# Kernel tuning notes

Measured on AMD Instinct MI355X. Metric: run time of the kernel, lower is better.

Reference implementation:

```python
import jax, jax.numpy as jnp
import numpy as np

N = 32768; D = 384; P = 3; CORR_D = 2 * 49 * P * P  # 882
G_KK = 4096; G_JK = 512
EPS = 1e-3  # LayerNorm eps in the torch module

FLOAT_NAMES = ("net","inp","corr","corr_w1","corr_b1","corr_w2","corr_b2","corr_ln_g","corr_ln_b","corr_w3","corr_b3","norm_g","norm_b","c1_w1","c1_b1","c1_w2","c1_b2","c2_w1","c2_b1","c2_w2","c2_b2","kk_fw","kk_fb","kk_gw","kk_gb","kk_hw","kk_hb","ij_fw","ij_fb","ij_gw","ij_gb","ij_hw","ij_hb","g_ln1_g","g_ln1_b","g1_gw","g1_gb","g1_r1w","g1_r1b","g1_r2w","g1_r2b","g_ln2_g","g_ln2_b","g2_gw","g2_gb","g2_r1w","g2_r1b","g2_r2w","g2_r2b","d_w","d_b","w_w","w_b")

def _ln(x, g, b):
    m = jnp.mean(x, -1, keepdims=True)
    v = jnp.mean((x - m) ** 2, -1, keepdims=True)
    return (x - m) * jax.lax.rsqrt(v + EPS) * g + b

def _mlp2(x, w1, b1, w2, b2):
    return jax.nn.relu(x @ w1 + b1) @ w2 + b2

def _gated_residual(x, gw, gb, r1w, r1b, r2w, r2b):
    gate = jax.nn.sigmoid(x @ gw + gb)
    res = jax.nn.relu(x @ r1w + r1b) @ r2w + r2b
    return x + gate * res

def _soft_agg(x, jx, fw, fb, gw, gb, hw, hb, num_groups):
    # x: [N, D]; jx: [N] group ids -> group-wise softmax weighted sum
    logits = x @ gw + gb
    feats = x @ fw + fb
    gmax = jax.ops.segment_max(logits, jx, num_segments=num_groups)
    e = jnp.exp(logits - gmax[jx])
    den = jax.ops.segment_sum(e, jx, num_segments=num_groups)
    w = e / (den[jx] + 1e-12)
    y = jax.ops.segment_sum(feats * w, jx, num_segments=num_groups)
    return (y @ hw + hb)[jx]

def _forward(p, nix, njx, ukk, ujk):
    # corr encoder MLP
    h = jax.nn.relu(p["corr"] @ p["corr_w1"] + p["corr_b1"]) @ p["corr_w2"] + p["corr_b2"]
    h = jax.nn.relu(_ln(h, p["corr_ln_g"], p["corr_ln_b"])) @ p["corr_w3"] + p["corr_b3"]
    net = p["net"] + p["inp"] + h
    net = _ln(net, p["norm_g"], p["norm_b"])
    mask_ix = (nix >= 0).astype(net.dtype).reshape(1, -1, 1)
    mask_jx = (njx >= 0).astype(net.dtype).reshape(1, -1, 1)
    net = net + _mlp2(mask_ix * net[:, nix], p["c1_w1"], p["c1_b1"], p["c1_w2"], p["c1_b2"])
    net = net + _mlp2(mask_jx * net[:, njx], p["c2_w1"], p["c2_b1"], p["c2_w2"], p["c2_b2"])
    net = net + _soft_agg(net[0], ukk, p["kk_fw"], p["kk_fb"], p["kk_gw"], p["kk_gb"], p["kk_hw"], p["kk_hb"], G_KK)[None]
    net = net + _soft_agg(net[0], ujk, p["ij_fw"], p["ij_fb"], p["ij_gw"], p["ij_gb"], p["ij_hw"], p["ij_hb"], G_JK)[None]
    net = _ln(net, p["g_ln1_g"], p["g_ln1_b"])
    net = _gated_residual(net, p["g1_gw"], p["g1_gb"], p["g1_r1w"], p["g1_r1b"], p["g1_r2w"], p["g1_r2b"])
    net = _ln(net, p["g_ln2_g"], p["g_ln2_b"])
    net = _gated_residual(net, p["g2_gw"], p["g2_gb"], p["g2_r1w"], p["g2_r1b"], p["g2_r2w"], p["g2_r2b"])
    r = jax.nn.relu(net)
    d = r @ p["d_w"] + p["d_b"]               # GradClip is identity in forward
    w = jax.nn.sigmoid(r @ p["w_w"] + p["w_b"])
    return net, d, w

def setup_inputs() -> dict:
    key = jax.random.key(0)
    it = iter(jax.random.split(key, 64))
    def pr(*shape):
        return jax.random.normal(next(it), shape, dtype=jnp.float32) * 0.02
    z = lambda *s: jnp.zeros(s, jnp.float32)
    o = lambda *s: jnp.ones(s, jnp.float32)
    inp = {
        "net": jax.random.normal(next(it), (1, N, D), dtype=jnp.float32),
        "inp": jax.random.normal(next(it), (1, N, D), dtype=jnp.float32),
        "corr": jax.random.normal(next(it), (1, N, CORR_D), dtype=jnp.float32),
        "nix": jax.random.randint(next(it), (N,), 0, N),
        "njx": jax.random.randint(next(it), (N,), 0, N),
        "ukk": jax.random.randint(next(it), (N,), 0, G_KK),
        "ujk": jax.random.randint(next(it), (N,), 0, G_JK),
        "corr_w1": pr(CORR_D, D), "corr_b1": z(D), "corr_w2": pr(D, D), "corr_b2": z(D),
        "corr_ln_g": o(D), "corr_ln_b": z(D), "corr_w3": pr(D, D), "corr_b3": z(D),
        "norm_g": o(D), "norm_b": z(D),
        "c1_w1": pr(D, D), "c1_b1": z(D), "c1_w2": pr(D, D), "c1_b2": z(D),
        "c2_w1": pr(D, D), "c2_b1": z(D), "c2_w2": pr(D, D), "c2_b2": z(D),
        "kk_fw": pr(D, D), "kk_fb": z(D), "kk_gw": pr(D, D), "kk_gb": z(D), "kk_hw": pr(D, D), "kk_hb": z(D),
        "ij_fw": pr(D, D), "ij_fb": z(D), "ij_gw": pr(D, D), "ij_gb": z(D), "ij_hw": pr(D, D), "ij_hb": z(D),
        "g_ln1_g": o(D), "g_ln1_b": z(D),
        "g1_gw": pr(D, D), "g1_gb": z(D), "g1_r1w": pr(D, D), "g1_r1b": z(D), "g1_r2w": pr(D, D), "g1_r2b": z(D),
        "g_ln2_g": o(D), "g_ln2_b": z(D),
        "g2_gw": pr(D, D), "g2_gb": z(D), "g2_r1w": pr(D, D), "g2_r1b": z(D), "g2_r2w": pr(D, D), "g2_r2b": z(D),
        "d_w": pr(D, 2), "d_b": z(2), "w_w": pr(D, 2), "w_b": z(2),
    }
    return inp

def reference(net, inp, corr, corr_w1, corr_b1, corr_w2, corr_b2, corr_ln_g, corr_ln_b, corr_w3, corr_b3, norm_g, norm_b, c1_w1, c1_b1, c1_w2, c1_b2, c2_w1, c2_b1, c2_w2, c2_b2, kk_fw, kk_fb, kk_gw, kk_gb, kk_hw, kk_hb, ij_fw, ij_fb, ij_gw, ij_gb, ij_hw, ij_hb, g_ln1_g, g_ln1_b, g1_gw, g1_gb, g1_r1w, g1_r1b, g1_r2w, g1_r2b, g_ln2_g, g_ln2_b, g2_gw, g2_gb, g2_r1w, g2_r1b, g2_r2w, g2_r2b, d_w, d_b, w_w, w_b, nix, njx, ukk, ujk):
    loc = locals()
    fl = {k: loc[k] for k in FLOAT_NAMES}
    return _forward(fl, nix, njx, ukk, ujk)
```

## Files before the change

### kernel.cpp

```cpp
#include <hip/hip_runtime.h>
#include <hip/hip_bf16.h>
#include <math.h>

#define NR 32768
#define DD 384
#define CDM 882
#define CDMP 896

typedef float f4 __attribute__((ext_vector_type(4)));
typedef float f32x4 __attribute__((ext_vector_type(4)));
typedef __bf16 bf16x8 __attribute__((ext_vector_type(8)));

__device__ inline f4 ld4(const float* p) { f4 v; __builtin_memcpy(&v, p, 16); return v; }
__device__ inline void st4(float* p, f4 v) { __builtin_memcpy(p, &v, 16); }
__device__ inline bf16x8 ld8h(const __bf16* p) { bf16x8 v; __builtin_memcpy(&v, p, 16); return v; }
__device__ inline void st8h(__bf16* p, bf16x8 v) { __builtin_memcpy(p, &v, 16); }

__device__ inline void gl_lds16(const void* g, void* l) {
  __builtin_amdgcn_global_load_lds(
      (const __attribute__((address_space(1))) void*)g,
      (__attribute__((address_space(3))) void*)l, 16, 0, 0);
}

__device__ inline float gred16(float v) {
#pragma unroll
  for (int o = 1; o < 16; o <<= 1) v += __shfl_xor(v, o, 64);
  return v;
}

__device__ inline int xcd_swz(int orig, int nwg) {
  int q = nwg >> 3, r = nwg & 7, xcd = orig & 7, lid = orig >> 3;
  return (xcd < r ? xcd * (q + 1) : r * (q + 1) + (xcd - r) * q) + lid;
}

struct WPtrs { const float* w[19]; };

__global__ __launch_bounds__(256) void trans_all_k(WPtrs P, __bf16* __restrict__ dst) {
  int wi = blockIdx.y;
  const float* W = P.w[wi];
  int i = blockIdx.x * 256 + threadIdx.x;
  if (wi < 18) {
    if (i >= DD * DD) return;
    int n = i / DD, k = i - n * DD;
    dst[(size_t)wi * DD * DD + i] = (__bf16)W[(size_t)k * DD + n];
  } else {
    if (i >= DD * CDMP) return;
    int n = i / CDMP, k = i - n * CDMP;
    dst[(size_t)18 * DD * DD + i] = (k < CDM) ? (__bf16)W[(size_t)k * DD + n] : (__bf16)0.f;
  }
}

struct GP {
  const void* A; const __bf16* WT; const float* bias; __bf16* OUT;
  const __bf16* XRES; const __bf16* GIN;
  const float* p0; const float* p1; const float* p2; const float* p3;
  float* fout; const float* net32; const float* inp32;
  const int* idx; const __bf16* zpage; int M; int K; int Kr;
};

template <int EPI>
__device__ __forceinline__ void epilogue(const GP& gp, f32x4 (&acc)[4][6],
                                         __bf16* sm, int m0, int w, int lane) {
  const int fr = lane & 15, fq = lane >> 4;
  const int wr = (w >> 2) * 64, wc = (w & 3) * 96;
  const int nw = w & 3;
  float bcol[6];
#pragma unroll
  for (int ni = 0; ni < 6; ++ni) bcol[ni] = gp.bias[wc + ni * 16 + fr];
#pragma unroll
  for (int mi = 0; mi < 4; ++mi)
#pragma unroll
    for (int ni = 0; ni < 6; ++ni)
#pragma unroll
      for (int j = 0; j < 4; ++j) acc[mi][ni][j] += bcol[ni];

  if constexpr (EPI <= 2) {
#pragma unroll
    for (int mi = 0; mi < 4; ++mi)
#pragma unroll
      for (int ni = 0; ni < 6; ++ni) {
        int col = wc + ni * 16 + fr;
#pragma unroll
        for (int j = 0; j < 4; ++j) {
          int row = m0 + wr + mi * 16 + fq * 4 + j;
          size_t o = (size_t)row * DD + col;
          float v = acc[mi][ni][j];
          if constexpr (EPI == 0) gp.OUT[o] = (__bf16)v;
          else if constexpr (EPI == 1) gp.OUT[o] = (__bf16)fmaxf(v, 0.f);
          else gp.OUT[o] = (__bf16)((float)gp.XRES[o] + v);
        }
      }
  } else {
    if constexpr (EPI == 5) {
#pragma unroll
      for (int mi = 0; mi < 4; ++mi)
#pragma unroll
        for (int ni = 0; ni < 6; ++ni) {
          int col = wc + ni * 16 + fr;
#pragma unroll
          for (int j = 0; j < 4; ++j) {
            int row = m0 + wr + mi * 16 + fq * 4 + j;
            size_t o = (size_t)row * DD + col;
            acc[mi][ni][j] += gp.net32[o] + gp.inp32[o];
          }
        }
    }
    if constexpr (EPI == 6 || EPI == 7) {
#pragma unroll
      for (int mi = 0; mi < 4; ++mi)
#pragma unroll
        for (int ni = 0; ni < 6; ++ni) {
          int col = wc + ni * 16 + fr;
#pragma unroll
          for (int j = 0; j < 4; ++j) {
            int row = m0 + wr + mi * 16 + fq * 4 + j;
            size_t o = (size_t)row * DD + col;
            float gl = (float)gp.GIN[o];
            float sg = 1.f / (1.f + expf(-gl));
            acc[mi][ni][j] = (float)gp.XRES[o] + sg * acc[mi][ni][j];
          }
        }
    }
    __syncthreads();
    if constexpr (EPI != 7) {
      float s1[4][4], s2[4][4];
#pragma unroll
      for (int mi = 0; mi < 4; ++mi)
#pragma unroll
        for (int j = 0; j < 4; ++j) { s1[mi][j] = 0.f; s2[mi][j] = 0.f; }
#pragma unroll
      for (int mi = 0; mi < 4; ++mi)
#pragma unroll
        for (int ni = 0; ni < 6; ++ni)
#pragma unroll
          for (int j = 0; j < 4; ++j) {
            float v = acc[mi][ni][j];
            s1[mi][j] += v;
            s2[mi][j] += v * v;
          }
#pragma unroll
      for (int o = 1; o < 16; o <<= 1)
#pragma unroll
        for (int mi = 0; mi < 4; ++mi)
#pragma unroll
          for (int j = 0; j < 4; ++j) {
            s1[mi][j] += __shfl_xor(s1[mi][j], o, 64);
            s2[mi][j] += __shfl_xor(s2[mi][j], o, 64);
          }
      float* lsum = (float*)sm;
      float* lsq = lsum + 512;
      if (fr == 0) {
#pragma unroll
        for (int mi = 0; mi < 4; ++mi)
#pragma unroll
          for (int j = 0; j < 4; ++j) {
            int rr = wr + mi * 16 + fq * 4 + j;
            lsum[rr * 4 + nw] = s1[mi][j];
            lsq[rr * 4 + nw] = s2[mi][j];
          }
      }
      __syncthreads();
      float mn[4][4], rs[4][4];
#pragma unroll
      for (int mi = 0; mi < 4; ++mi)
#pragma unroll
        for (int j = 0; j < 4; ++j) {
          int rr = wr + mi * 16 + fq * 4 + j;
          float S1 = lsum[rr * 4] + lsum[rr * 4 + 1] + lsum[rr * 4 + 2] + lsum[rr * 4 + 3];
          float S2 = lsq[rr * 4] + lsq[rr * 4 + 1] + lsq[rr * 4 + 2] + lsq[rr * 4 + 3];
          float m = S1 * (1.f / 384.f);
          float va = S2 * (1.f / 384.f) - m * m;
          mn[mi][j] = m;
          rs[mi][j] = rsqrtf(va + 1e-3f);
        }
#pragma unroll
      for (int ni = 0; ni < 6; ++ni) {
        int col = wc + ni * 16 + fr;
        float gg = gp.p0[col], bb = gp.p1[col];
#pragma unroll
        for (int mi = 0; mi < 4; ++mi)
#pragma unroll
          for (int j = 0; j < 4; ++j) {
            int row = m0 + wr + mi * 16 + fq * 4 + j;
            float y = (acc[mi][ni][j] - mn[mi][j]) * rs[mi][j] * gg + bb;
            if constexpr (EPI == 4) y = fmaxf(y, 0.f);
            gp.OUT[(size_t)row * DD + col] = (__bf16)y;
          }
      }
    } else {
      float c0[6], c1[6], c2[6], c3[6];
#pragma unroll
      for (int ni = 0; ni < 6; ++ni) {
        int col = wc + ni * 16 + fr;
        c0[ni] = gp.p0[2 * col];
        c1[ni] = gp.p0[2 * col + 1];
        c2[ni] = gp.p2[2 * col];
        c3[ni] = gp.p2[2 * col + 1];
      }
      float dt[4][4][4];
#pragma unroll
      for (int mi = 0; mi < 4; ++mi)
#pragma unroll
        for (int j = 0; j < 4; ++j)
#pragma unroll
          for (int q = 0; q < 4; ++q) dt[mi][j][q] = 0.f;
#pragma unroll
      for (int mi = 0; mi < 4; ++mi)
#pragma unroll
        for (int ni = 0; ni < 6; ++ni) {
          int col = wc + ni * 16 + fr;
#pragma unroll
          for (int j = 0; j < 4; ++j) {
            int row = m0 + wr + mi * 16 + fq * 4 + j;
            float v = acc[mi][ni][j];
            gp.fout[(size_t)row * DD + col] = v;
            float r = fmaxf(v, 0.f);
            dt[mi][j][0] += r * c0[ni];
            dt[mi][j][1] += r * c1[ni];
            dt[mi][j][2] += r * c2[ni];
            dt[mi][j][3] += r * c3[ni];
          }
        }
#pragma unroll
      for (int o = 1; o < 16; o <<= 1)
#pragma unroll
        for (int mi = 0; mi < 4; ++mi)
#pragma unroll
          for (int j = 0; j < 4; ++j)
#pragma unroll
            for (int q = 0; q < 4; ++q)
              dt[mi][j][q] += __shfl_xor(dt[mi][j][q], o, 64);
      float* lt = (float*)sm;
      if (fr == 0) {
#pragma unroll
        for (int mi = 0; mi < 4; ++mi)
#pragma unroll
          for (int j = 0; j < 4; ++j) {
            int rr = wr + mi * 16 + fq * 4 + j;
#pragma unroll
            for (int q = 0; q < 4; ++q) lt[(rr * 4 + nw) * 4 + q] = dt[mi][j][q];
          }
      }
      __syncthreads();
      if (nw == 0 && fr == 0) {
        float* fd = gp.fout + (size_t)NR * DD;
        float* fw = fd + (size_t)NR * 2;
#pragma unroll
        for (int mi = 0; mi < 4; ++mi)
#pragma unroll
          for (int j = 0; j < 4; ++j) {
            int rr = wr + mi * 16 + fq * 4 + j;
            int row = m0 + rr;
            float T[4];
#pragma unroll
            for (int q = 0; q < 4; ++q)
              T[q] = lt[(rr * 4 + 0) * 4 + q] + lt[(rr * 4 + 1) * 4 + q] +
                     lt[(rr * 4 + 2) * 4 + q] + lt[(rr * 4 + 3) * 4 + q];
            fd[2 * row] = T[0] + gp.p1[0];
            fd[2 * row + 1] = T[1] + gp.p1[1];
            fw[2 * row] = 1.f / (1.f + expf(-(T[2] + gp.p3[0])));
            fw[2 * row + 1] = 1.f / (1.f + expf(-(T[3] + gp.p3[1])));
          }
      }
    }
  }
}

__device__ __forceinline__ void mfma_block(const __bf16* As, const __bf16* Bs,
                                           f32x4 (&acc)[4][6], int wr, int wc,
                                           int fr, int fq) {
#pragma unroll
  for (int kk2 = 0; kk2 < 2; ++kk2) {
    bf16x8 af[4];
    bf16x8 bv[6];
#pragma unroll
    for (int mi = 0; mi < 4; ++mi) {
      int rr = wr + mi * 16 + fr;
      af[mi] = *reinterpret_cast<const bf16x8*>(
          &As[rr * 64 + (((fq + kk2 * 4) ^ (rr & 7)) << 3)]);
    }
#pragma unroll
    for (int ni = 0; ni < 6; ++ni) {
      int rr = wc + ni * 16 + fr;
      bv[ni] = *reinterpret_cast<const bf16x8*>(
          &Bs[rr * 64 + (((fq + kk2 * 4) ^ (rr & 7)) << 3)]);
    }
#pragma unroll
    for (int mi = 0; mi < 4; ++mi)
#pragma unroll
      for (int ni = 0; ni < 6; ++ni)
        acc[mi][ni] = __builtin_amdgcn_mfma_f32_16x16x32_bf16(af[mi], bv[ni],
                                                              acc[mi][ni], 0, 0, 0);
  }
}

__device__ __forceinline__ void zero_acc(f32x4 (&acc)[4][6]) {
#pragma unroll
  for (int a = 0; a < 4; ++a)
#pragma unroll
    for (int b = 0; b < 6; ++b)
#pragma unroll
      for (int j = 0; j < 4; ++j) acc[a][b][j] = 0.f;
}

__device__ __forceinline__ void phase1_run(const GP& gp, f32x4 (&acc)[4][6],
                                           __bf16* sm, int m0, int t, int w,
                                           int lane, int NT) {
  const int fr = lane & 15, fq = lane >> 4;
  const int wr = (w >> 2) * 64, wc = (w & 3) * 96;
  const int K = gp.K;
  const __bf16* aptr[2];
  int aadv[2];
  const __bf16* bptr[6];
#pragma unroll
  for (int j = 0; j < 2; ++j) {
    int rloc = w * 16 + j * 8 + (lane >> 3);
    int cch = (lane & 7) ^ (rloc & 7);
    int ar = gp.idx ? gp.idx[m0 + rloc] : (m0 + rloc);
    if (ar >= 0) { aptr[j] = (const __bf16*)gp.A + (size_t)ar * K + cch * 8; aadv[j] = 64; }
    else { aptr[j] = gp.zpage; aadv[j] = 0; }
  }
#pragma unroll
  for (int j = 0; j < 6; ++j) {
    int rloc = w * 48 + j * 8 + (lane >> 3);
    int cch = (lane & 7) ^ (rloc & 7);
    bptr[j] = gp.WT + (size_t)rloc * K + cch * 8;
  }
  auto stageG = [&](int buf) {
    __bf16* As = sm + buf * 32768;
    __bf16* Bs = As + 8192;
#pragma unroll
    for (int j = 0; j < 2; ++j) {
      gl_lds16(aptr[j], &As[(w * 16 + j * 8) * 64]);
      aptr[j] += aadv[j];
    }
#pragma unroll
    for (int j = 0; j < 6; ++j) {
      gl_lds16(bptr[j], &Bs[(w * 48 + j * 8) * 64]);
      bptr[j] += 64;
    }
  };
  stageG(0);
  int buf = 0;
  for (int tt = 0; tt < NT; ++tt) {
    if (tt + 1 < NT) {
      stageG(buf ^ 1);
      asm volatile("s_waitcnt vmcnt(8)" ::: "memory");
    } else {
      asm volatile("s_waitcnt vmcnt(0)" ::: "memory");
    }
    __builtin_amdgcn_s_barrier();
    __builtin_amdgcn_sched_barrier(0);
    mfma_block(sm + buf * 32768, sm + buf * 32768 + 8192, acc, wr, wc, fr, fq);
    __builtin_amdgcn_s_barrier();
    __builtin_amdgcn_sched_barrier(0);
    buf ^= 1;
  }
}

template <int EPI, int AFP32>
__global__ __launch_bounds__(512, 1) void gemm_k(GP gp) {
  __shared__ __align__(16) __bf16 sm[2 * 32768];
  const int t = threadIdx.x;
  const int w = t >> 6, lane = t & 63;
  const int m0 = xcd_swz(blockIdx.x, gridDim.x) * 128;
  const int fr = lane & 15, fq = lane >> 4;
  const int wr = (w >> 2) * 64, wc = (w & 3) * 96;
  f32x4 acc[4][6];
  zero_acc(acc);
  if constexpr (AFP32) {
    const float* Af = (const float*)gp.A;
    const int K = gp.K, Kr = gp.Kr;
    const __bf16* bptr[6];
#pragma unroll
    for (int j = 0; j < 6; ++j) {
      int rloc = w * 48 + j * 8 + (lane >> 3);
      int cch = (lane & 7) ^ (rloc & 7);
      bptr[j] = gp.WT + (size_t)rloc * K + cch * 8;
    }
    const int NT = K >> 6;
    for (int tt = 0; tt < NT; ++tt) {
      if (tt) __syncthreads();
      __bf16* As = sm;
      __bf16* Bs = sm + 8192;
#pragma unroll
      for (int j = 0; j < 2; ++j) {
        int rr = (t >> 3) + 64 * j;
        int cc = t & 7;
        int kb = (tt << 6) + cc * 8;
        const float* ap = Af + (size_t)(m0 + rr) * Kr + kb;
        bf16x8 h;
        if (kb + 8 <= Kr) {
          f4 v0 = ld4(ap), v1 = ld4(ap + 4);
#pragma unroll
          for (int e = 0; e < 4; ++e) { h[e] = (__bf16)v0[e]; h[4 + e] = (__bf16)v1[e]; }
        } else {
#pragma unroll
          for (int e = 0; e < 8; ++e) h[e] = (kb + e < Kr) ? (__bf16)ap[e] : (__bf16)0.f;
        }
        *reinterpret_cast<bf16x8*>(&As[rr * 64 + ((cc ^ (rr & 7)) << 3)]) = h;
      }
#pragma unroll
      for (int j = 0; j < 6; ++j) {
        gl_lds16(bptr[j], &Bs[(w * 48 + j * 8) * 64]);
        bptr[j] += 64;
      }
      __syncthreads();
      mfma_block(sm, sm + 8192, acc, wr, wc, fr, fq);
    }
  } else {
    phase1_run(gp, acc, sm, m0, t, w, lane, gp.K >> 6);
  }
  epilogue<EPI>(gp, acc, sm, m0, w, lane);
}

template <int EPIA, int EPIB>
__global__ __launch_bounds__(512, 1) void gemm2_k(GP ga, GP gb) {
  __shared__ __align__(16) __bf16 sm[2 * 32768];
  const int t = threadIdx.x;
  const int w = t >> 6, lane = t & 63;
  int wg = xcd_swz(blockIdx.x, gridDim.x);
  const int role = wg >> 8;
  const int m0 = (wg & 255) * 128;
  const GP& gp = role ? gb : ga;
  f32x4 acc[4][6];
  zero_acc(acc);
  phase1_run(gp, acc, sm, m0, t, w, lane, gp.K >> 6);
  if (role == 0) epilogue<EPIA>(ga, acc, sm, m0, w, lane);
  else epilogue<EPIB>(gb, acc, sm, m0, w, lane);
}

__global__ __launch_bounds__(256) void ln_ag_k(const __bf16* __restrict__ X,
                                               const __bf16* __restrict__ z,
                                               const int* __restrict__ gid,
                                               const float* __restrict__ g,
                                               const float* __restrict__ b,
                                               __bf16* __restrict__ out) {
  int w = threadIdx.x >> 6, lane = threadIdx.x & 63;
  int s = lane & 15, qq = lane >> 4;
  int row = blockIdx.x * 16 + w * 4 + qq;
  int gr = gid[row];
  size_t base = (size_t)row * DD;
  size_t zbase = (size_t)gr * DD;
  float v[24];
#pragma unroll
  for (int i = 0; i < 3; ++i) {
    int col = (s + 16 * i) * 8;
    bf16x8 h = ld8h(X + base + col);
    bf16x8 zz = ld8h(z + zbase + col);
#pragma unroll
    for (int e = 0; e < 8; ++e) v[i * 8 + e] = (float)h[e] + (float)zz[e];
  }
  float sm = 0.f;
#pragma unroll
  for (int i = 0; i < 24; ++i) sm += v[i];
  sm = gred16(sm);
  float mean = sm * (1.f / 384.f);
  float qs = 0.f;
#pragma unroll
  for (int i = 0; i < 24; ++i) { float d = v[i] - mean; qs += d * d; }
  qs = gred16(qs);
  float rs = rsqrtf(qs * (1.f / 384.f) + 1e-3f);
#pragma unroll
  for (int i = 0; i < 3; ++i) {
    int col = (s + 16 * i) * 8;
    f4 g0 = ld4(g + col), g1 = ld4(g + col + 4);
    f4 b0 = ld4(b + col), b1 = ld4(b + col + 4);
    bf16x8 o;
#pragma unroll
    for (int e = 0; e < 4; ++e) {
      o[e] = (__bf16)((v[i * 8 + e] - mean) * rs * g0[e] + b0[e]);
      o[4 + e] = (__bf16)((v[i * 8 + 4 + e] - mean) * rs * g1[e] + b1[e]);
    }
    st8h(out + base + col, o);
  }
}

__global__ __launch_bounds__(256) void hist2_k(const int* __restrict__ ukk,
                                               const int* __restrict__ ujk,
                                               int* __restrict__ ckk,
                                               int* __restrict__ cij) {
  int i = blockIdx.x * 256 + threadIdx.x;
  atomicAdd(&ckk[ukk[i]], 1);
  atomicAdd(&cij[ujk[i]], 1);
}

__device__ inline void scan_body(const int* cnt, int* off, int* curb, int G, int* ls) {
  int t = threadIdx.x;
  int per = G / 256;
  int base = t * per;
  int s = 0;
  for (int i = 0; i < per; ++i) s += cnt[base + i];
  ls[t] = s;
  __syncthreads();
  for (int o = 1; o < 256; o <<= 1) {
    int v = (t >= o) ? ls[t - o] : 0;
    __syncthreads();
    ls[t] += v;
    __syncthreads();
  }
  int run = (t == 0) ? 0 : ls[t - 1];
  for (int i = 0; i < per; ++i) {
    off[base + i] = run;
    run += cnt[base + i];
    curb[base + i] = 0;
  }
  if (t == 255) off[G] = run;
}

__global__ __launch_bounds__(256) void scan2_k(const int* ckk, int* okk, int* qkk,
                                               const int* cij, int* oij, int* qij) {
  __shared__ int ls[256];
  if (blockIdx.x == 0) scan_body(ckk, okk, qkk, 4096, ls);
  else scan_body(cij, oij, qij, 512, ls);
}

__global__ __launch_bounds__(256) void scatter2_k(const int* __restrict__ ukk,
                                                  const int* __restrict__ ujk,
                                                  const int* __restrict__ okk,
                                                  int* __restrict__ qkk,
                                                  int* __restrict__ rkk,
                                                  const int* __restrict__ oij,
                                                  int* __restrict__ qij,
                                                  int* __restrict__ rij) {
  int i = blockIdx.x * 256 + threadIdx.x;
  int g1 = ukk[i];
  rkk[okk[g1] + atomicAdd(&qkk[g1], 1)] = i;
  int g2 = ujk[i];
  rij[oij[g2] + atomicAdd(&qij[g2], 1)] = i;
}

__global__ __launch_bounds__(384) void segagg_k(const __bf16* __restrict__ L,
                                                const __bf16* __restrict__ Ft,
                                                const int* __restrict__ rows,
                                                const int* __restrict__ off,
                                                float* __restrict__ yb) {
  int g = blockIdx.x;
  int c = threadIdx.x;
  int s = off[g], e = off[g + 1];
  float mx = -3.0e38f;
  for (int p = s; p < e; ++p) {
    int r = rows[p];
    mx = fmaxf(mx, (float)L[(size_t)r * DD + c]);
  }
  float num = 0.f, den = 0.f;
  for (int p = s; p < e; ++p) {
    int r = rows[p];
    float lv = (float)L[(size_t)r * DD + c];
    float fv = (float)Ft[(size_t)r * DD + c];
    float ev = expf(lv - mx);
    den += ev;
    num += fv * ev;
  }
  yb[(size_t)g * DD + c] = num / (den + 1e-12f);
}

__global__ __launch_bounds__(256) void addgather_k(__bf16* __restrict__ X,
                                                   const __bf16* __restrict__ z,
                                                   const int* __restrict__ gid) {
  int i = blockIdx.x * 256 + threadIdx.x;
  int row = i / 48, c = (i - row * 48) * 8;
  int g = gid[row];
  size_t lo = (size_t)row * DD + c;
  bf16x8 a = ld8h(X + lo);
  bf16x8 zz = ld8h(z + (size_t)g * DD + c);
  bf16x8 o;
#pragma unroll
  for (int e = 0; e < 8; ++e) o[e] = (__bf16)((float)a[e] + (float)zz[e]);
  st8h(X + lo, o);
}

extern "C" void kernel_launch(void* const* d_in, const int* in_sizes, int n_in,
                              void* d_out, int out_size, void* d_ws, size_t ws_size,
                              hipStream_t stream) {
  const float* in_net = (const float*)d_in[0];
  const float* in_inp = (const float*)d_in[1];
  const float* in_corr = (const float*)d_in[2];
  const int* nix = (const int*)d_in[3];
  const int* njx = (const int*)d_in[4];
  const int* ukk = (const int*)d_in[5];
  const int* ujk = (const int*)d_in[6];
  auto F = [&](int i) { return (const float*)d_in[i]; };

  constexpr size_t MiB = 1024 * 1024;
  constexpr size_t SZ_ACT = (size_t)NR * DD * 2;
  char* ws = (char*)d_ws;
  __bf16* T2b = (__bf16*)(ws);
  __bf16* Fb = (__bf16*)(ws + SZ_ACT);
  __bf16* zb = (__bf16*)(ws + 2 * SZ_ACT);
  float* yb = (float*)(ws + 2 * SZ_ACT + 3 * MiB);
  __bf16* T1b = (__bf16*)(ws + 60 * MiB);
  char* p = ws + 84 * MiB;
  int* rows_kk = (int*)p; p += (size_t)NR * 4;
  int* rows_ij = (int*)p; p += (size_t)NR * 4;
  int* off_kk = (int*)p; p += 8192 * 4;
  int* off_ij = (int*)p; p += 1024 * 4;
  int* cnt_kk = (int*)p; p += 4096 * 4;
  int* cnt_ij = (int*)p; p += 512 * 4;
  int* curb_kk = (int*)p; p += 4096 * 4;
  int* curb_ij = (int*)p; p += 512 * 4;
  __bf16* wt_all = (__bf16*)p; p += (size_t)18 * DD * DD * 2;
  __bf16* wt_corr1 = (__bf16*)p; p += (size_t)DD * CDMP * 2;
  __bf16* zpage = (__bf16*)p;

  const int widx[18] = {17, 19, 21, 23, 25, 27, 29, 31, 33, 35, 39, 41, 43, 47, 49, 51, 9, 13};
  WPtrs P;
  for (int i = 0; i < 18; ++i) P.w[i] = F(widx[i]);
  P.w[18] = F(7);
  auto WTp = [&](int i) { return wt_all + (size_t)i * DD * DD; };

  hipMemsetAsync(zpage, 0, 256, stream);
  hipMemsetAsync(cnt_kk, 0, 4096 * 4, stream);
  hipMemsetAsync(cnt_ij, 0, 512 * 4, stream);
  trans_all_k<<<dim3(1344, 19), 256, 0, stream>>>(P, wt_all);
  hist2_k<<<NR / 256, 256, 0, stream>>>(ukk, ujk, cnt_kk, cnt_ij);
  scan2_k<<<2, 256, 0, stream>>>(cnt_kk, off_kk, curb_kk, cnt_ij, off_ij, curb_ij);
  scatter2_k<<<NR / 256, 256, 0, stream>>>(ukk, ujk, off_kk, curb_kk, rows_kk,
                                           off_ij, curb_ij, rows_ij);

  auto mkGP = [&]() {
    GP g{};
    g.zpage = zpage;
    g.K = DD;
    g.Kr = DD;
    g.M = NR;
    return g;
  };

  auto launch = [&](int epi, int afp32, const GP& gp) {
    dim3 g(gp.M / 128), b(512);
    if (afp32) {
      if (epi == 1) gemm_k<1, 1><<<g, b, 0, stream>>>(gp);
      else gemm_k<0, 1><<<g, b, 0, stream>>>(gp);
      return;
    }
    switch (epi) {
      case 0: gemm_k<0, 0><<<g, b, 0, stream>>>(gp); break;
      case 1: gemm_k<1, 0><<<g, b, 0, stream>>>(gp); break;
      case 2: gemm_k<2, 0><<<g, b, 0, stream>>>(gp); break;
      case 4: gemm_k<4, 0><<<g, b, 0, stream>>>(gp); break;
      case 5: gemm_k<5, 0><<<g, b, 0, stream>>>(gp); break;
      case 6: gemm_k<6, 0><<<g, b, 0, stream>>>(gp); break;
      case 7: gemm_k<7, 0><<<g, b, 0, stream>>>(gp); break;
    }
  };
  auto launch2 = [&](int epib, const GP& ga, const GP& gb) {
    dim3 g(512), b(512);
    if (epib == 0) gemm2_k<0, 0><<<g, b, 0, stream>>>(ga, gb);
    else gemm2_k<0, 1><<<g, b, 0, stream>>>(ga, gb);
  };

  const int SEGB = NR * 48 / 256;

  {
    GP g = mkGP(); g.A = in_corr; g.WT = wt_corr1; g.bias = F(8); g.OUT = T1b;
    g.K = CDMP; g.Kr = CDM;
    launch(1, 1, g);
  }
  {
    GP g = mkGP(); g.A = T1b; g.WT = WTp(16); g.bias = F(10); g.OUT = T2b;
    g.p0 = F(11); g.p1 = F(12);
    launch(4, 0, g);
  }
  {
    GP g = mkGP(); g.A = T2b; g.WT = WTp(17); g.bias = F(14); g.OUT = T1b;
    g.p0 = F(15); g.p1 = F(16); g.net32 = in_net; g.inp32 = in_inp;
    launch(5, 0, g);
  }
  {
    GP g = mkGP(); g.A = T1b; g.WT = WTp(0); g.bias = F(18); g.OUT = T2b; g.idx = nix;
    launch(1, 0, g);
  }
  {
    GP g = mkGP(); g.A = T2b; g.WT = WTp(1); g.bias = F(20); g.OUT = Fb; g.XRES = T1b;
    launch(2, 0, g);
  }
  {
    GP g = mkGP(); g.A = Fb; g.WT = WTp(2); g.bias = F(22); g.OUT = T2b; g.idx = njx;
    launch(1, 0, g);
  }
  {
    GP g = mkGP(); g.A = T2b; g.WT = WTp(3); g.bias = F(24); g.OUT = T1b; g.XRES = Fb;
    launch(2, 0, g);
  }
  {
    GP ga = mkGP(); ga.A = T1b; ga.WT = WTp(5); ga.bias = F(28); ga.OUT = T2b;
    GP gb = mkGP(); gb.A = T1b; gb.WT = WTp(4); gb.bias = F(26); gb.OUT = Fb;
    launch2(0, ga, gb);
  }
  segagg_k<<<4096, 384, 0, stream>>>(T2b, Fb, rows_kk, off_kk, yb);
  {
    GP g = mkGP(); g.A = yb; g.WT = WTp(6); g.bias = F(30); g.OUT = zb; g.M = 4096;
    launch(0, 1, g);
  }
  addgather_k<<<SEGB, 256, 0, stream>>>(T1b, zb, ukk);
  {
    GP ga = mkGP(); ga.A = T1b; ga.WT = WTp(8); ga.bias = F(34); ga.OUT = T2b;
    GP gb = mkGP(); gb.A = T1b; gb.WT = WTp(7); gb.bias = F(32); gb.OUT = Fb;
    launch2(0, ga, gb);
  }
  segagg_k<<<512, 384, 0, stream>>>(T2b, Fb, rows_ij, off_ij, yb);
  {
    GP g = mkGP(); g.A = yb; g.WT = WTp(9); g.bias = F(36); g.OUT = zb; g.M = 512;
    launch(0, 1, g);
  }
  ln_ag_k<<<NR / 16, 256, 0, stream>>>(T1b, zb, ujk, F(37), F(38), T2b);
  {
    GP ga = mkGP(); ga.A = T2b; ga.WT = WTp(10); ga.bias = F(40); ga.OUT = Fb;
    GP gb = mkGP(); gb.A = T2b; gb.WT = WTp(11); gb.bias = F(42); gb.OUT = T1b;
    launch2(1, ga, gb);
  }
  {
    GP g = mkGP(); g.A = T1b; g.WT = WTp(12); g.bias = F(44); g.OUT = T2b;
    g.XRES = T2b; g.GIN = Fb; g.p0 = F(45); g.p1 = F(46);
    launch(6, 0, g);
  }
  {
    GP ga = mkGP(); ga.A = T2b; ga.WT = WTp(13); ga.bias = F(48); ga.OUT = Fb;
    GP gb = mkGP(); gb.A = T2b; gb.WT = WTp(14); gb.bias = F(50); gb.OUT = T1b;
    launch2(1, ga, gb);
  }
  {
    GP g = mkGP(); g.A = T1b; g.WT = WTp(15); g.bias = F(52);
    g.XRES = T2b; g.GIN = Fb; g.p0 = F(53); g.p1 = F(54); g.p2 = F(55); g.p3 = F(56);
    g.fout = (float*)d_out;
    launch(7, 0, g);
  }
}
```

Baseline: 628.4 us.

## Stage residual/gate tiles through LDS, precompute net+inp, split dual GEMM launches

Adds a kernel that sums net and inp into one bf16 buffer, so the corr-encoder epilogue reads a single bf16 residual instead of two fp32 tensors. Residual and gate epilogues now copy the tile into LDS with async global-to-LDS loads rather than doing strided per-element global reads, and the LayerNorm epilogue is restructured. The fused two-role gemm2 kernel is removed and replaced by two sequential single GEMM launches. This adds an extra elementwise pass and extra launches in exchange for more coalesced epilogue traffic.

```diff
diff --git a/kernel.cpp b/kernel.cpp
--- a/kernel.cpp
+++ b/kernel.cpp
@@ -12,7 +12,6 @@
 typedef __bf16 bf16x8 __attribute__((ext_vector_type(8)));
 
 __device__ inline f4 ld4(const float* p) { f4 v; __builtin_memcpy(&v, p, 16); return v; }
-__device__ inline void st4(float* p, f4 v) { __builtin_memcpy(p, &v, 16); }
 __device__ inline bf16x8 ld8h(const __bf16* p) { bf16x8 v; __builtin_memcpy(&v, p, 16); return v; }
 __device__ inline void st8h(__bf16* p, bf16x8 v) { __builtin_memcpy(p, &v, 16); }
 
@@ -31,6 +30,21 @@
 __device__ inline int xcd_swz(int orig, int nwg) {
   int q = nwg >> 3, r = nwg & 7, xcd = orig & 7, lid = orig >> 3;
   return (xcd < r ? xcd * (q + 1) : r * (q + 1) + (xcd - r) * q) + lid;
+}
+
+__global__ __launch_bounds__(256) void ni_k(const float* __restrict__ a,
+                                            const float* __restrict__ b,
+                                            __bf16* __restrict__ o) {
+  size_t base = ((size_t)blockIdx.x * 256 + threadIdx.x) * 8;
+  f4 a0 = ld4(a + base), a1 = ld4(a + base + 4);
+  f4 b0 = ld4(b + base), b1 = ld4(b + base + 4);
+  bf16x8 h;
+#pragma unroll
+  for (int e = 0; e < 4; ++e) {
+    h[e] = (__bf16)(a0[e] + b0[e]);
+    h[4 + e] = (__bf16)(a1[e] + b1[e]);
+  }
+  st8h(o + base, h);
 }
 
 struct WPtrs { const float* w[19]; };
@@ -54,13 +68,24 @@
   const void* A; const __bf16* WT; const float* bias; __bf16* OUT;
   const __bf16* XRES; const __bf16* GIN;
   const float* p0; const float* p1; const float* p2; const float* p3;
-  float* fout; const float* net32; const float* inp32;
-  const int* idx; const __bf16* zpage; int M; int K; int Kr;
+  float* fout; const int* idx; const __bf16* zpage; int M; int K; int Kr;
 };
+
+__device__ __forceinline__ void stage_tile(const __bf16* X, int m0, __bf16* sm, int t) {
+  const char* src = (const char*)(X + (size_t)m0 * DD);
+  char* dst = (char*)sm;
+#pragma unroll
+  for (int i = 0; i < 12; ++i) {
+    int ch = t + i * 512;
+    gl_lds16(src + (size_t)ch * 16, dst + ch * 16);
+  }
+  asm volatile("s_waitcnt vmcnt(0)" ::: "memory");
+  __builtin_amdgcn_s_barrier();
+}
 
 template <int EPI>
 __device__ __forceinline__ void epilogue(const GP& gp, f32x4 (&acc)[4][6],
-                                         __bf16* sm, int m0, int w, int lane) {
+                                         __bf16* sm, int m0, int w, int lane, int t) {
   const int fr = lane & 15, fq = lane >> 4;
   const int wr = (w >> 2) * 64, wc = (w & 3) * 96;
   const int nw = w & 3;
@@ -74,7 +99,7 @@
 #pragma unroll
       for (int j = 0; j < 4; ++j) acc[mi][ni][j] += bcol[ni];
 
-  if constexpr (EPI <= 2) {
+  if constexpr (EPI <= 1) {
 #pragma unroll
     for (int mi = 0; mi < 4; ++mi)
 #pragma unroll
@@ -86,43 +111,111 @@
           size_t o = (size_t)row * DD + col;
           float v = acc[mi][ni][j];
           if constexpr (EPI == 0) gp.OUT[o] = (__bf16)v;
-          else if constexpr (EPI == 1) gp.OUT[o] = (__bf16)fmaxf(v, 0.f);
-          else gp.OUT[o] = (__bf16)((float)gp.XRES[o] + v);
-        }
-      }
-  } else {
-    if constexpr (EPI == 5) {
-#pragma unroll
-      for (int mi = 0; mi < 4; ++mi)
+          else gp.OUT[o] = (__bf16)fmaxf(v, 0.f);
+        }
+      }
+  } else if constexpr (EPI == 4) {
+    __syncthreads();
+    float s1[4][4], s2[4][4];
+#pragma unroll
+    for (int mi = 0; mi < 4; ++mi)
+#pragma unroll
+      for (int j = 0; j < 4; ++j) { s1[mi][j] = 0.f; s2[mi][j] = 0.f; }
+#pragma unroll
+    for (int mi = 0; mi < 4; ++mi)
+#pragma unroll
+      for (int ni = 0; ni < 6; ++ni)
+#pragma unroll
+        for (int j = 0; j < 4; ++j) {
+          float v = acc[mi][ni][j];
+          s1[mi][j] += v;
+          s2[mi][j] += v * v;
+        }
+#pragma unroll
+    for (int o = 1; o < 16; o <<= 1)
+#pragma unroll
+      for (int mi = 0; mi < 4; ++mi)
+#pragma unroll
+        for (int j = 0; j < 4; ++j) {
+          s1[mi][j] += __shfl_xor(s1[mi][j], o, 64);
+          s2[mi][j] += __shfl_xor(s2[mi][j], o, 64);
+        }
+    float* lsum = (float*)sm;
+    float* lsq = lsum + 512;
+    if (fr == 0) {
+#pragma unroll
+      for (int mi = 0; mi < 4; ++mi)
+#pragma unroll
+        for (int j = 0; j < 4; ++j) {
+          int rr = wr + mi * 16 + fq * 4 + j;
+          lsum[rr * 4 + nw] = s1[mi][j];
+          lsq[rr * 4 + nw] = s2[mi][j];
+        }
+    }
+    __syncthreads();
+#pragma unroll
+    for (int mi = 0; mi < 4; ++mi)
+#pragma unroll
+      for (int j = 0; j < 4; ++j) {
+        int rr = wr + mi * 16 + fq * 4 + j;
+        float S1 = lsum[rr * 4] + lsum[rr * 4 + 1] + lsum[rr * 4 + 2] + lsum[rr * 4 + 3];
+        float S2 = lsq[rr * 4] + lsq[rr * 4 + 1] + lsq[rr * 4 + 2] + lsq[rr * 4 + 3];
+        float m = S1 * (1.f / 384.f);
+        float va = S2 * (1.f / 384.f) - m * m;
+        float rs = rsqrtf(va + 1e-3f);
 #pragma unroll
         for (int ni = 0; ni < 6; ++ni) {
           int col = wc + ni * 16 + fr;
+          float y = (acc[mi][ni][j] - m) * rs * gp.p0[col] + gp.p1[col];
+          gp.OUT[(size_t)(m0 + rr) * DD + col] = (__bf16)fmaxf(y, 0.f);
+        }
+      }
+  } else {
+    __syncthreads();
+    if constexpr (EPI == 6 || EPI == 7) {
+      stage_tile(gp.GIN, m0, sm, t);
+#pragma unroll
+      for (int mi = 0; mi < 4; ++mi)
+#pragma unroll
+        for (int ni = 0; ni < 6; ++ni) {
+          int col = wc + ni * 16 + fr;
+#pragma unroll
+          for (int j = 0; j < 4; ++j) {
+            int rr = wr + mi * 16 + fq * 4 + j;
+            float gl = (float)sm[rr * DD + col];
+            acc[mi][ni][j] *= 1.f / (1.f + expf(-gl));
+          }
+        }
+      __syncthreads();
+    }
+    stage_tile(gp.XRES, m0, sm, t);
+#pragma unroll
+    for (int mi = 0; mi < 4; ++mi)
+#pragma unroll
+      for (int ni = 0; ni < 6; ++ni) {
+        int col = wc + ni * 16 + fr;
+#pragma unroll
+        for (int j = 0; j < 4; ++j) {
+          int rr = wr + mi * 16 + fq * 4 + j;
+          acc[mi][ni][j] += (float)sm[rr * DD + col];
+        }
+      }
+    if constexpr (EPI == 2) {
+#pragma unroll
+      for (int mi = 0; mi < 4; ++mi)
+#pragma unroll
+        for (int ni = 0; ni < 6; ++ni) {
+          int col = wc + ni * 16 + fr;
 #pragma unroll
           for (int j = 0; j < 4; ++j) {
             int row = m0 + wr + mi * 16 + fq * 4 + j;
-            size_t o = (size_t)row * DD + col;
-            acc[mi][ni][j] += gp.net32[o] + gp.inp32[o];
-          }
-        }
-    }
-    if constexpr (EPI == 6 || EPI == 7) {
-#pragma unroll
-      for (int mi = 0; mi < 4; ++mi)
-#pragma unroll
-        for (int ni = 0; ni < 6; ++ni) {
-          int col = wc + ni * 16 + fr;
-#pragma unroll
-          for (int j = 0; j < 4; ++j) {
-            int row = m0 + wr + mi * 16 + fq * 4 + j;
-            size_t o = (size_t)row * DD + col;
-            float gl = (float)gp.GIN[o];
-            float sg = 1.f / (1.f + expf(-gl));
-            acc[mi][ni][j] = (float)gp.XRES[o] + sg * acc[mi][ni][j];
-          }
-        }
+            gp.OUT[(size_t)row * DD + col] = (__bf16)acc[mi][ni][j];
+          }
+        }
+      return;
     }
     __syncthreads();
-    if constexpr (EPI != 7) {
+    if constexpr (EPI == 5 || EPI == 6) {
       float s1[4][4], s2[4][4];
 #pragma unroll
       for (int mi = 0; mi < 4; ++mi)
@@ -160,7 +253,6 @@
           }
       }
       __syncthreads();
-      float mn[4][4], rs[4][4];
 #pragma unroll
       for (int mi = 0; mi < 4; ++mi)
 #pragma unroll
@@ -170,23 +262,14 @@
           float S2 = lsq[rr * 4] + lsq[rr * 4 + 1] + lsq[rr * 4 + 2] + lsq[rr * 4 + 3];
           float m = S1 * (1.f / 384.f);
           float va = S2 * (1.f / 384.f) - m * m;
-          mn[mi][j] = m;
-          rs[mi][j] = rsqrtf(va + 1e-3f);
-        }
-#pragma unroll
-      for (int ni = 0; ni < 6; ++ni) {
-        int col = wc + ni * 16 + fr;
-        float gg = gp.p0[col], bb = gp.p1[col];
-#pragma unroll
-        for (int mi = 0; mi < 4; ++mi)
-#pragma unroll
-          for (int j = 0; j < 4; ++j) {
-            int row = m0 + wr + mi * 16 + fq * 4 + j;
-            float y = (acc[mi][ni][j] - mn[mi][j]) * rs[mi][j] * gg + bb;
-            if constexpr (EPI == 4) y = fmaxf(y, 0.f);
-            gp.OUT[(size_t)row * DD + col] = (__bf16)y;
-          }
-      }
+          float rs = rsqrtf(va + 1e-3f);
+#pragma unroll
+          for (int ni = 0; ni < 6; ++ni) {
+            int col = wc + ni * 16 + fr;
+            float y = (acc[mi][ni][j] - m) * rs * gp.p0[col] + gp.p1[col];
+            gp.OUT[(size_t)(m0 + rr) * DD + col] = (__bf16)y;
+          }
+        }
     } else {
       float c0[6], c1[6], c2[6], c3[6];
 #pragma unroll
@@ -408,26 +491,11 @@
       __syncthreads();
       mfma_block(sm, sm + 8192, acc, wr, wc, fr, fq);
     }
+    __syncthreads();
   } else {
     phase1_run(gp, acc, sm, m0, t, w, lane, gp.K >> 6);
   }
-  epilogue<EPI>(gp, acc, sm, m0, w, lane);
-}
-
-template <int EPIA, int EPIB>
-__global__ __launch_bounds__(512, 1) void gemm2_k(GP ga, GP gb) {
-  __shared__ __align__(16) __bf16 sm[2 * 32768];
-  const int t = threadIdx.x;
-  const int w = t >> 6, lane = t & 63;
-  int wg = xcd_swz(blockIdx.x, gridDim.x);
-  const int role = wg >> 8;
-  const int m0 = (wg & 255) * 128;
-  const GP& gp = role ? gb : ga;
-  f32x4 acc[4][6];
-  zero_acc(acc);
-  phase1_run(gp, acc, sm, m0, t, w, lane, gp.K >> 6);
-  if (role == 0) epilogue<EPIA>(ga, acc, sm, m0, w, lane);
-  else epilogue<EPIB>(gb, acc, sm, m0, w, lane);
+  epilogue<EPI>(gp, acc, sm, m0, w, lane, t);
 }
 
 __global__ __launch_bounds__(256) void ln_ag_k(const __bf16* __restrict__ X,
@@ -601,7 +669,8 @@
   int* curb_ij = (int*)p; p += 512 * 4;
   __bf16* wt_all = (__bf16*)p; p += (size_t)18 * DD * DD * 2;
   __bf16* wt_corr1 = (__bf16*)p; p += (size_t)DD * CDMP * 2;
-  __bf16* zpage = (__bf16*)p;
+  __bf16* zpage = (__bf16*)p; p += 4096;
+  __bf16* NI = (__bf16*)p;
 
   const int widx[18] = {17, 19, 21, 23, 25, 27, 29, 31, 33, 35, 39, 41, 43, 47, 49, 51, 9, 13};
   WPtrs P;
@@ -613,6 +682,7 @@
   hipMemsetAsync(cnt_kk, 0, 4096 * 4, stream);
   hipMemsetAsync(cnt_ij, 0, 512 * 4, stream);
   trans_all_k<<<dim3(1344, 19), 256, 0, stream>>>(P, wt_all);
+  ni_k<<<NR * DD / 8 / 256, 256, 0, stream>>>(in_net, in_inp, NI);
   hist2_k<<<NR / 256, 256, 0, stream>>>(ukk, ujk, cnt_kk, cnt_ij);
   scan2_k<<<2, 256, 0, stream>>>(cnt_kk, off_kk, curb_kk, cnt_ij, off_ij, curb_ij);
   scatter2_k<<<NR / 256, 256, 0, stream>>>(ukk, ujk, off_kk, curb_kk, rows_kk,
@@ -644,11 +714,6 @@
       case 7: gemm_k<7, 0><<<g, b, 0, stream>>>(gp); break;
     }
   };
-  auto launch2 = [&](int epib, const GP& ga, const GP& gb) {
-    dim3 g(512), b(512);
-    if (epib == 0) gemm2_k<0, 0><<<g, b, 0, stream>>>(ga, gb);
-    else gemm2_k<0, 1><<<g, b, 0, stream>>>(ga, gb);
-  };
 
   const int SEGB = NR * 48 / 256;
 
@@ -664,7 +729,7 @@
   }
   {
     GP g = mkGP(); g.A = T2b; g.WT = WTp(17); g.bias = F(14); g.OUT = T1b;
-    g.p0 = F(15); g.p1 = F(16); g.net32 = in_net; g.inp32 = in_inp;
+    g.p0 = F(15); g.p1 = F(16); g.XRES = NI;
     launch(5, 0, g);
   }
   {
@@ -684,9 +749,10 @@
     launch(2, 0, g);
   }
   {
-    GP ga = mkGP(); ga.A = T1b; ga.WT = WTp(5); ga.bias = F(28); ga.OUT = T2b;
-    GP gb = mkGP(); gb.A = T1b; gb.WT = WTp(4); gb.bias = F(26); gb.OUT = Fb;
-    launch2(0, ga, gb);
+    GP g = mkGP(); g.A = T1b; g.WT = WTp(5); g.bias = F(28); g.OUT = T2b;
+    launch(0, 0, g);
+    g.WT = WTp(4); g.bias = F(26); g.OUT = Fb;
+    launch(0, 0, g);
   }
   segagg_k<<<4096, 384, 0, stream>>>(T2b, Fb, rows_kk, off_kk, yb);
   {
@@ -695,9 +761,10 @@
   }
   addgather_k<<<SEGB, 256, 0, stream>>>(T1b, zb, ukk);
   {
-    GP ga = mkGP(); ga.A = T1b; ga.WT = WTp(8); ga.bias = F(34); ga.OUT = T2b;
-    GP gb = mkGP(); gb.A = T1b; gb.WT = WTp(7); gb.bias = F(32); gb.OUT = Fb;
-    launch2(0, ga, gb);
+    GP g = mkGP(); g.A = T1b; g.WT = WTp(8); g.bias = F(34); g.OUT = T2b;
+    launch(0, 0, g);
+    g.WT = WTp(7); g.bias = F(32); g.OUT = Fb;
+    launch(0, 0, g);
   }
   segagg_k<<<512, 384, 0, stream>>>(T2b, Fb, rows_ij, off_ij, yb);
   {
@@ -706,9 +773,10 @@
   }
   ln_ag_k<<<NR / 16, 256, 0, stream>>>(T1b, zb, ujk, F(37), F(38), T2b);
   {
-    GP ga = mkGP(); ga.A = T2b; ga.WT = WTp(10); ga.bias = F(40); ga.OUT = Fb;
-    GP gb = mkGP(); gb.A = T2b; gb.WT = WTp(11); gb.bias = F(42); gb.OUT = T1b;
-    launch2(1, ga, gb);
+    GP g = mkGP(); g.A = T2b; g.WT = WTp(10); g.bias = F(40); g.OUT = Fb;
+    launch(0, 0, g);
+    g.WT = WTp(11); g.bias = F(42); g.OUT = T1b;
+    launch(1, 0, g);
   }
   {
     GP g = mkGP(); g.A = T1b; g.WT = WTp(12); g.bias = F(44); g.OUT = T2b;
@@ -716,9 +784,10 @@
     launch(6, 0, g);
   }
   {
-    GP ga = mkGP(); ga.A = T2b; ga.WT = WTp(13); ga.bias = F(48); ga.OUT = Fb;
-    GP gb = mkGP(); gb.A = T2b; gb.WT = WTp(14); gb.bias = F(50); gb.OUT = T1b;
-    launch2(1, ga, gb);
+    GP g = mkGP(); g.A = T2b; g.WT = WTp(13); g.bias = F(48); g.OUT = Fb;
+    launch(0, 0, g);
+    g.WT = WTp(14); g.bias = F(50); g.OUT = T1b;
+    launch(1, 0, g);
   }
   {
     GP g = mkGP(); g.A = T1b; g.WT = WTp(15); g.bias = F(52);
```

New measurement: 651.9 us. +3.7%, slower.
